# Kernel tuning notes

Measured on AMD Instinct MI355X. Metric: run time of the kernel, lower is better.

## Reference

```python
import jax, jax.numpy as jnp
import numpy as np

E = 32        # num_local_experts
TOP_K = 4     # num_experts_per_tok
H = 1024      # hidden_size
I = 1024      # intermediate_size (expert_dim)
ALPHA = 1.702
LIMIT = 7.0
B, S = 2, 1024


def setup_inputs() -> dict:
    key = jax.random.key(0)
    ks = jax.random.split(key, 8)
    scale = 0.02
    return {
        "hidden_states": jax.random.normal(ks[0], (B, S, H), dtype=jnp.float32),
        "gate_up_proj": jax.random.normal(ks[1], (E, H, 2 * I), dtype=jnp.float32) * scale,
        "gate_up_proj_bias": jax.random.normal(ks[2], (E, 2 * I), dtype=jnp.float32) * scale,
        "down_proj": jax.random.normal(ks[3], (E, I, H), dtype=jnp.float32) * scale,
        "down_proj_bias": jax.random.normal(ks[4], (E, H), dtype=jnp.float32) * scale,
        "router_weight": jax.random.normal(ks[5], (E, H), dtype=jnp.float32) * scale,
        "router_bias": jax.random.normal(ks[6], (E,), dtype=jnp.float32) * scale,
    }


def reference(hidden_states, gate_up_proj, gate_up_proj_bias, down_proj,
              down_proj_bias, router_weight, router_bias):
    b, s, h = hidden_states.shape
    x = hidden_states.reshape(-1, h)                       # [T, H], T = B*S
    t = x.shape[0]

    # ---- router: linear -> topk -> softmax over topk -> scatter to dense scores
    router_logits = x @ router_weight.T + router_bias      # [T, E]
    top_vals, top_idx = jax.lax.top_k(router_logits, TOP_K)
    top_w = jax.nn.softmax(top_vals, axis=-1)
    router_scores = jnp.zeros_like(router_logits).at[
        jnp.arange(t)[:, None], top_idx].set(top_w)        # [T, E]

    # ---- experts (dense all-expert path, interleaved gate/up columns)
    gate_w = gate_up_proj[..., 0::2]                       # [E, H, I]
    up_w = gate_up_proj[..., 1::2]                         # [E, H, I]
    gate_b = gate_up_proj_bias[..., 0::2]                  # [E, I]
    up_b = gate_up_proj_bias[..., 1::2]                    # [E, I]

    gate = jnp.einsum('th,ehi->eti', x, gate_w) + gate_b[:, None, :]
    up = jnp.einsum('th,ehi->eti', x, up_w) + up_b[:, None, :]
    gate = jnp.minimum(gate, LIMIT)
    up = jnp.clip(up, -LIMIT, LIMIT)
    glu = gate * jax.nn.sigmoid(gate * ALPHA)
    next_states = jnp.einsum('eti,eih->eth', (up + 1.0) * glu, down_proj)
    next_states = next_states + down_proj_bias[:, None, :]  # [E, T, H]

    # ---- combine: weight each expert output by its routing score and sum
    routed = jnp.einsum('eth,te->th', next_states, router_scores)
    return routed.reshape(b, s, h), router_scores
```

## Files before the change

kernel.cpp:

```cpp
#include <hip/hip_runtime.h>
#include <cstdint>
#include <cstddef>

#define E_ 32
#define TOPK_ 4
#define H_ 1024
#define I_ 1024
#define T_ 2048
#define ALPHA_ 1.702f
#define LIMIT_ 7.0f
#define TP_ 66
#define NCH_ 32

typedef __attribute__((ext_vector_type(8))) short s8;
typedef __attribute__((ext_vector_type(4))) float f4;

__device__ __forceinline__ unsigned short f2bf(float f) {
  unsigned int u = __float_as_uint(f);
  return (unsigned short)((u + 0x7fffu + ((u >> 16) & 1u)) >> 16);
}

__device__ __forceinline__ void gload_lds16(const unsigned short* g,
                                            unsigned short* l) {
  __builtin_amdgcn_global_load_lds(
      (const __attribute__((address_space(1))) void*)g,
      (__attribute__((address_space(3))) void*)l, 16, 0, 0);
}

__global__ __launch_bounds__(256)
void cast_x_kernel(const float* __restrict__ x, unsigned short* __restrict__ xb) {
  size_t i = (size_t)(blockIdx.x * 256 + threadIdx.x) * 8;
  float4 a = *(const float4*)(x + i);
  float4 b = *(const float4*)(x + i + 4);
  s8 v;
  v[0] = (short)f2bf(a.x); v[1] = (short)f2bf(a.y);
  v[2] = (short)f2bf(a.z); v[3] = (short)f2bf(a.w);
  v[4] = (short)f2bf(b.x); v[5] = (short)f2bf(b.y);
  v[6] = (short)f2bf(b.z); v[7] = (short)f2bf(b.w);
  *(s8*)(xb + i) = v;
}

__global__ __launch_bounds__(256)
void transpose_cast(const float* __restrict__ src, unsigned short* __restrict__ dst,
                    int src_rows, int src_cols, int deint) {
  int e = blockIdx.z;
  int c0 = blockIdx.x * 64;
  int r0 = blockIdx.y * 64;
  int tid = threadIdx.x;
  __shared__ unsigned short ldsT[64][TP_];

  const float* sp = src + (size_t)e * src_rows * src_cols
                        + (size_t)r0 * src_cols + c0;
  int r = tid >> 2, cq = tid & 3;
  const float* rowp = sp + (size_t)r * src_cols + cq * 4;
  #pragma unroll
  for (int j = 0; j < 4; ++j) {
    float4 v = *(const float4*)(rowp + j * 16);
    int c = cq * 4 + j * 16;
    ldsT[c + 0][r] = f2bf(v.x);
    ldsT[c + 1][r] = f2bf(v.y);
    ldsT[c + 2][r] = f2bf(v.z);
    ldsT[c + 3][r] = f2bf(v.w);
  }
  __syncthreads();

  int co = tid >> 2, hq = tid & 3;
  s8 v0 = *(s8*)&ldsT[co][hq * 16];
  s8 v1 = *(s8*)&ldsT[co][hq * 16 + 8];
  int C = c0 + co;
  size_t out_off;
  if (deint) {
    out_off = (size_t)e * src_cols * src_rows
            + (size_t)(C & 1) * (src_cols >> 1) * src_rows
            + (size_t)(C >> 1) * src_rows + r0 + hq * 16;
  } else {
    out_off = (size_t)e * src_cols * src_rows
            + (size_t)C * src_rows + r0 + hq * 16;
  }
  *(s8*)(dst + out_off) = v0;
  *(s8*)(dst + out_off + 8) = v1;
}

__global__ __launch_bounds__(128)
void router_kernel(const float* __restrict__ x,
                   const float* __restrict__ rw,
                   const float* __restrict__ rb,
                   float* __restrict__ scores,
                   int* __restrict__ counts,
                   int* __restrict__ tok_list,
                   float* __restrict__ w_list) {
  int t = blockIdx.x;
  int tid = threadIdx.x;
  __shared__ float partial[128];
  __shared__ float logits[E_];
  int e = tid & 31, q = tid >> 5;
  const float4* xp = (const float4*)(x + (size_t)t * H_ + q * 256);
  const float4* wp = (const float4*)(rw + (size_t)e * H_ + q * 256);
  float s = 0.f;
  #pragma unroll 8
  for (int h = 0; h < 64; ++h) {
    float4 a = xp[h], b = wp[h];
    s += a.x * b.x + a.y * b.y + a.z * b.z + a.w * b.w;
  }
  partial[tid] = s;
  __syncthreads();
  if (tid < 32)
    logits[tid] = partial[tid] + partial[tid + 32] + partial[tid + 64] +
                  partial[tid + 96] + rb[tid];
  __syncthreads();
  if (tid == 0) {
    float l[E_];
    #pragma unroll
    for (int i = 0; i < E_; ++i) l[i] = logits[i];
    int idx[TOPK_]; float v[TOPK_];
    for (int k = 0; k < TOPK_; ++k) {
      int bi = 0; float bv = -1e30f;
      for (int i = 0; i < E_; ++i)
        if (l[i] > bv) { bv = l[i]; bi = i; }
      idx[k] = bi; v[k] = bv; l[bi] = -1e30f;
    }
    float m = v[0], den = 0.f, w[TOPK_];
    for (int k = 0; k < TOPK_; ++k) { w[k] = expf(v[k] - m); den += w[k]; }
    float inv = 1.f / den;
    float* srow = scores + (size_t)t * E_;
    #pragma unroll
    for (int i = 0; i < E_; ++i) srow[i] = 0.f;
    for (int k = 0; k < TOPK_; ++k) {
      float wk = w[k] * inv;
      srow[idx[k]] = wk;
      int pos = atomicAdd(&counts[idx[k]], 1);
      tok_list[idx[k] * T_ + pos] = t * TOPK_ + k;
      w_list[idx[k] * T_ + pos] = wk;
    }
  }
}

__global__ __launch_bounds__(256)
void gateup_mfma(const unsigned short* __restrict__ xb,
                 const unsigned short* __restrict__ wgu,
                 const float* __restrict__ gb,
                 const int* __restrict__ counts,
                 const int* __restrict__ tok_list,
                 unsigned short* __restrict__ act) {
  int lid = blockIdx.x;
  int xcd = lid & 7, s = lid >> 3;
  int e = (xcd << 2) + (s >> 7);
  int w = s & 127;
  int tblk = w & 7;
  int itile = w >> 3;

  int cnt = counts[e];
  int t0 = tblk * 64;
  if (t0 >= cnt) return;
  int tid = threadIdx.x;
  int lane = tid & 63;
  int wave = tid >> 6;
  int wm = wave >> 1, wn = wave & 1;

  __shared__ __align__(16) unsigned short Xs[2][64][32];
  __shared__ __align__(16) unsigned short Wg[2][128][32];
  __shared__ int toks[64];

  if (tid < 64) {
    int slot = t0 + tid;
    toks[tid] = (slot < cnt) ? tok_list[e * T_ + slot] : -1;
  }
  __syncthreads();

  int fm = lane & 15, ko = (lane >> 4) * 8;
  f4 accg[2][2] = {};
  f4 accu[2][2] = {};

  int arow = (wave << 4) + (lane >> 2);
  int aenc_l = toks[arow];
  const unsigned short* srcA =
      xb + (size_t)((aenc_l < 0) ? 0 : (aenc_l >> 2)) * H_ + ((lane & 3) << 3);
  int br0 = (wave << 5) + (lane >> 2);
  int br1 = br0 + 16;
  size_t R0 = (br0 < 64) ? (size_t)(itile * 64 + br0)
                         : (size_t)(I_ + itile * 64 + (br0 - 64));
  size_t R1 = (br1 < 64) ? (size_t)(itile * 64 + br1)
                         : (size_t)(I_ + itile * 64 + (br1 - 64));
  const unsigned short* wbase = wgu + (size_t)e * 2 * I_ * H_ + ((lane & 3) << 3);
  const unsigned short* srcB0 = wbase + R0 * H_;
  const unsigned short* srcB1 = wbase + R1 * H_;

#define GU_ISSUE(CC, P)                                                      \
  {                                                                          \
    gload_lds16(srcA + (size_t)(CC) * 32, &Xs[P][wave << 4][0]);             \
    gload_lds16(srcB0 + (size_t)(CC) * 32, &Wg[P][wave << 5][0]);            \
    gload_lds16(srcB1 + (size_t)(CC) * 32, &Wg[P][(wave << 5) + 16][0]);     \
  }

  GU_ISSUE(0, 0)
  GU_ISSUE(1, 1)
  asm volatile("s_waitcnt vmcnt(3)" ::: "memory");
  __builtin_amdgcn_s_barrier();
  asm volatile("" ::: "memory");

  for (int c = 0; c < NCH_; ++c) {
    int P = c & 1;
    {
      s8 a0 = *(const s8*)&Xs[P][wm * 32 + fm][ko];
      s8 a1 = *(const s8*)&Xs[P][wm * 32 + 16 + fm][ko];
      #pragma unroll
      for (int g = 0; g < 2; ++g) {
        s8 bg = *(const s8*)&Wg[P][wn * 32 + g * 16 + fm][ko];
        s8 bu = *(const s8*)&Wg[P][64 + wn * 32 + g * 16 + fm][ko];
        accg[0][g] = __builtin_amdgcn_mfma_f32_16x16x32_bf16(a0, bg, accg[0][g], 0, 0, 0);
        accg[1][g] = __builtin_amdgcn_mfma_f32_16x16x32_bf16(a1, bg, accg[1][g], 0, 0, 0);
        accu[0][g] = __builtin_amdgcn_mfma_f32_16x16x32_bf16(a0, bu, accu[0][g], 0, 0, 0);
        accu[1][g] = __builtin_amdgcn_mfma_f32_16x16x32_bf16(a1, bu, accu[1][g], 0, 0, 0);
      }
    }
    __builtin_amdgcn_s_barrier();
    asm volatile("" ::: "memory");
    if (c < NCH_ - 2) {
      GU_ISSUE(c + 2, P)
      asm volatile("s_waitcnt vmcnt(3)" ::: "memory");
    } else if (c == NCH_ - 2) {
      asm volatile("s_waitcnt vmcnt(0)" ::: "memory");
    }
    __builtin_amdgcn_s_barrier();
    asm volatile("" ::: "memory");
  }
#undef GU_ISSUE

  int rq = lane >> 4;
  #pragma unroll
  for (int g = 0; g < 2; ++g) {
    int i = itile * 64 + wn * 32 + g * 16 + fm;
    float bg_ = gb[e * 2 * I_ + 2 * i];
    float bu_ = gb[e * 2 * I_ + 2 * i + 1];
    #pragma unroll
    for (int f = 0; f < 2; ++f) {
      #pragma unroll
      for (int r = 0; r < 4; ++r) {
        int m = wm * 32 + f * 16 + rq * 4 + r;
        int enc = toks[m];
        if (enc < 0) continue;
        float gv = accg[f][g][r] + bg_;
        float uv = accu[f][g][r] + bu_;
        gv = fminf(gv, LIMIT_);
        uv = fminf(fmaxf(uv, -LIMIT_), LIMIT_);
        float glu = gv / (1.f + __expf(-ALPHA_ * gv));
        act[(size_t)enc * I_ + i] = f2bf((uv + 1.f) * glu);
      }
    }
  }
}

__global__ __launch_bounds__(256)
void down_mfma(const unsigned short* __restrict__ act,
               const unsigned short* __restrict__ wdt,
               const float* __restrict__ db,
               const int* __restrict__ counts,
               const int* __restrict__ tok_list,
               const float* __restrict__ w_list,
               float* __restrict__ dsout) {
  int lid = blockIdx.x;
  int xcd = lid & 7, s = lid >> 3;
  int e = (xcd << 2) + (s >> 6);
  int w = s & 63;
  int tblk = w & 7;
  int htile = w >> 3;

  int cnt = counts[e];
  int t0 = tblk * 64;
  if (t0 >= cnt) return;
  int tid = threadIdx.x;
  int lane = tid & 63;
  int wave = tid >> 6;
  int wm = wave >> 1, wn = wave & 1;

  __shared__ __align__(16) unsigned short Xs[2][64][32];
  __shared__ __align__(16) unsigned short Wd[2][128][32];
  __shared__ int toks[64];
  __shared__ float tws[64];

  if (tid < 64) {
    int slot = t0 + tid;
    bool ok = slot < cnt;
    toks[tid] = ok ? tok_list[e * T_ + slot] : -1;
    tws[tid]  = ok ? w_list[e * T_ + slot] : 0.f;
  }
  __syncthreads();

  int fm = lane & 15, ko = (lane >> 4) * 8;
  f4 acc[2][4] = {};

  int arow = (wave << 4) + (lane >> 2);
  int aenc_l = toks[arow];
  const unsigned short* srcA =
      act + (size_t)((aenc_l < 0) ? 0 : aenc_l) * I_ + ((lane & 3) << 3);
  int br0 = (wave << 5) + (lane >> 2);
  int br1 = br0 + 16;
  const unsigned short* wbase = wdt + (size_t)e * H_ * I_ + ((lane & 3) << 3);
  const unsigned short* srcB0 = wbase + (size_t)(htile * 128 + br0) * I_;
  const unsigned short* srcB1 = wbase + (size_t)(htile * 128 + br1) * I_;

#define DN_ISSUE(CC, P)                                                      \
  {                                                                          \
    gload_lds16(srcA + (size_t)(CC) * 32, &Xs[P][wave << 4][0]);             \
    gload_lds16(srcB0 + (size_t)(CC) * 32, &Wd[P][wave << 5][0]);            \
    gload_lds16(srcB1 + (size_t)(CC) * 32, &Wd[P][(wave << 5) + 16][0]);     \
  }

  DN_ISSUE(0, 0)
  DN_ISSUE(1, 1)
  asm volatile("s_waitcnt vmcnt(3)" ::: "memory");
  __builtin_amdgcn_s_barrier();
  asm volatile("" ::: "memory");

  for (int c = 0; c < NCH_; ++c) {
    int P = c & 1;
    {
      s8 a0 = *(const s8*)&Xs[P][wm * 32 + fm][ko];
      s8 a1 = *(const s8*)&Xs[P][wm * 32 + 16 + fm][ko];
      #pragma unroll
      for (int g = 0; g < 4; ++g) {
        s8 b = *(const s8*)&Wd[P][wn * 64 + g * 16 + fm][ko];
        acc[0][g] = __builtin_amdgcn_mfma_f32_16x16x32_bf16(a0, b, acc[0][g], 0, 0, 0);
        acc[1][g] = __builtin_amdgcn_mfma_f32_16x16x32_bf16(a1, b, acc[1][g], 0, 0, 0);
      }
    }
    __builtin_amdgcn_s_barrier();
    asm volatile("" ::: "memory");
    if (c < NCH_ - 2) {
      DN_ISSUE(c + 2, P)
      asm volatile("s_waitcnt vmcnt(3)" ::: "memory");
    } else if (c == NCH_ - 2) {
      asm volatile("s_waitcnt vmcnt(0)" ::: "memory");
    }
    __builtin_amdgcn_s_barrier();
    asm volatile("" ::: "memory");
  }
#undef DN_ISSUE

  int rq = lane >> 4;
  #pragma unroll
  for (int g = 0; g < 4; ++g) {
    int h = htile * 128 + wn * 64 + g * 16 + fm;
    float bias = db[e * H_ + h];
    #pragma unroll
    for (int f = 0; f < 2; ++f) {
      #pragma unroll
      for (int r = 0; r < 4; ++r) {
        int m = wm * 32 + f * 16 + rq * 4 + r;
        int enc = toks[m];
        if (enc < 0) continue;
        dsout[(size_t)enc * H_ + h] = (acc[f][g][r] + bias) * tws[m];
      }
    }
  }
}

__global__ __launch_bounds__(256)
void combine_kernel(const float* __restrict__ dsout,
                    float* __restrict__ routed) {
  int idx = blockIdx.x * 256 + threadIdx.x;
  int t = idx >> 8;
  int h = (idx & 255) * 4;
  const float* base = dsout + (size_t)t * 4 * H_ + h;
  float4 a = *(const float4*)(base);
  float4 b = *(const float4*)(base + H_);
  float4 c = *(const float4*)(base + 2 * H_);
  float4 d = *(const float4*)(base + 3 * H_);
  float4 o;
  o.x = a.x + b.x + c.x + d.x;
  o.y = a.y + b.y + c.y + d.y;
  o.z = a.z + b.z + c.z + d.z;
  o.w = a.w + b.w + c.w + d.w;
  *(float4*)(routed + (size_t)t * H_ + h) = o;
}

extern "C" void kernel_launch(void* const* d_in, const int* in_sizes, int n_in,
                              void* d_out, int out_size, void* d_ws, size_t ws_size,
                              hipStream_t stream) {
  (void)in_sizes; (void)n_in; (void)out_size; (void)ws_size;
  const float* x    = (const float*)d_in[0];
  const float* gup  = (const float*)d_in[1];
  const float* gupb = (const float*)d_in[2];
  const float* dwn  = (const float*)d_in[3];
  const float* dwnb = (const float*)d_in[4];
  const float* rw   = (const float*)d_in[5];
  const float* rb   = (const float*)d_in[6];

  float* routed = (float*)d_out;
  float* scores = (float*)d_out + (size_t)T_ * H_;

  char* ws = (char*)d_ws;
  int*   counts   = (int*)ws;
  int*   tok_list = (int*)(ws + ((size_t)1 << 20));
  float* w_list   = (float*)(ws + ((size_t)1 << 20) + (size_t)E_ * T_ * 4);
  unsigned short* xbf = (unsigned short*)(ws + ((size_t)2 << 20));
  unsigned short* act = (unsigned short*)(ws + ((size_t)8 << 20));
  unsigned short* wgu_b = (unsigned short*)(ws + ((size_t)24 << 20));
  float*          dsout = (float*)(ws + ((size_t)24 << 20));
  unsigned short* wdt_b = (unsigned short*)(ws + ((size_t)24 << 20)
                                            + (size_t)E_ * 2 * I_ * H_ * 2);

  hipMemsetAsync(counts, 0, E_ * sizeof(int), stream);

  cast_x_kernel<<<(T_ * H_ / 8) / 256, 256, 0, stream>>>(x, xbf);
  transpose_cast<<<dim3(2 * I_ / 64, H_ / 64, E_), 256, 0, stream>>>(
      gup, wgu_b, H_, 2 * I_, 1);
  transpose_cast<<<dim3(H_ / 64, I_ / 64, E_), 256, 0, stream>>>(
      dwn, wdt_b, I_, H_, 0);
  router_kernel<<<T_, 128, 0, stream>>>(x, rw, rb, scores, counts, tok_list, w_list);
  gateup_mfma<<<4096, 256, 0, stream>>>(xbf, wgu_b, gupb, counts, tok_list, act);
  down_mfma<<<2048, 256, 0, stream>>>(act, wdt_b, dwnb, counts, tok_list,
                                      w_list, dsout);
  combine_kernel<<<(T_ * H_ / 4) / 256, 256, 0, stream>>>(dsout, routed);
}
```

Baseline: 738.0 us.

## Merge prep kernels, enlarge token tiles, swizzle LDS, atomically combine expert outputs

Router, x cast and both weight transposes now run as branches of a single prep kernel launch. The gate-up and down GEMMs use 128-token tiles instead of 64, with an XOR swizzle on LDS columns to reduce bank conflicts, and issue fewer blocks. The separate combine kernel is removed: the down kernel atomically adds weighted outputs into a zeroed output buffer. This cuts launch overhead and weight reloads, but adds atomic contention and makes the summation order nondeterministic. Also, with a max of 512 tokens per expert, any expert routed more than 512 tokens would be dropped.

```diff
diff --git a/kernel.cpp b/kernel.cpp
--- a/kernel.cpp
+++ b/kernel.cpp
@@ -12,6 +12,11 @@
 #define TP_ 66
 #define NCH_ 32
 
+#define NB_RTR_  2048
+#define NB_CAST_ 1024
+#define NB_TGUP_ 16384
+#define NB_TDWN_ 8192
+
 typedef __attribute__((ext_vector_type(8))) short s8;
 typedef __attribute__((ext_vector_type(4))) float f4;
 
@@ -27,28 +32,10 @@
       (__attribute__((address_space(3))) void*)l, 16, 0, 0);
 }
 
-__global__ __launch_bounds__(256)
-void cast_x_kernel(const float* __restrict__ x, unsigned short* __restrict__ xb) {
-  size_t i = (size_t)(blockIdx.x * 256 + threadIdx.x) * 8;
-  float4 a = *(const float4*)(x + i);
-  float4 b = *(const float4*)(x + i + 4);
-  s8 v;
-  v[0] = (short)f2bf(a.x); v[1] = (short)f2bf(a.y);
-  v[2] = (short)f2bf(a.z); v[3] = (short)f2bf(a.w);
-  v[4] = (short)f2bf(b.x); v[5] = (short)f2bf(b.y);
-  v[6] = (short)f2bf(b.z); v[7] = (short)f2bf(b.w);
-  *(s8*)(xb + i) = v;
-}
-
-__global__ __launch_bounds__(256)
-void transpose_cast(const float* __restrict__ src, unsigned short* __restrict__ dst,
-                    int src_rows, int src_cols, int deint) {
-  int e = blockIdx.z;
-  int c0 = blockIdx.x * 64;
-  int r0 = blockIdx.y * 64;
-  int tid = threadIdx.x;
-  __shared__ unsigned short ldsT[64][TP_];
-
+__device__ __forceinline__ void transpose_body(
+    const float* __restrict__ src, unsigned short* __restrict__ dst,
+    int src_rows, int src_cols, int deint, int e, int c0, int r0, int tid,
+    unsigned short (*ldsT)[TP_]) {
   const float* sp = src + (size_t)e * src_rows * src_cols
                         + (size_t)r0 * src_cols + c0;
   int r = tid >> 2, cq = tid & 3;
@@ -63,7 +50,6 @@
     ldsT[c + 3][r] = f2bf(v.w);
   }
   __syncthreads();
-
   int co = tid >> 2, hq = tid & 3;
   s8 v0 = *(s8*)&ldsT[co][hq * 16];
   s8 v1 = *(s8*)&ldsT[co][hq * 16 + 8];
@@ -81,57 +67,99 @@
   *(s8*)(dst + out_off + 8) = v1;
 }
 
-__global__ __launch_bounds__(128)
-void router_kernel(const float* __restrict__ x,
-                   const float* __restrict__ rw,
-                   const float* __restrict__ rb,
-                   float* __restrict__ scores,
-                   int* __restrict__ counts,
-                   int* __restrict__ tok_list,
-                   float* __restrict__ w_list) {
-  int t = blockIdx.x;
+__global__ __launch_bounds__(256)
+void prep_kernel(const float* __restrict__ x,
+                 const float* __restrict__ rw,
+                 const float* __restrict__ rb,
+                 const float* __restrict__ gup,
+                 const float* __restrict__ dwn,
+                 float* __restrict__ scores,
+                 int* __restrict__ counts,
+                 int* __restrict__ tok_list,
+                 float* __restrict__ w_list,
+                 unsigned short* __restrict__ xbf,
+                 unsigned short* __restrict__ wgu_b,
+                 unsigned short* __restrict__ wdt_b) {
+  __shared__ __align__(16) char smem[64 * TP_ * 2];
+  int bid = blockIdx.x;
   int tid = threadIdx.x;
-  __shared__ float partial[128];
-  __shared__ float logits[E_];
-  int e = tid & 31, q = tid >> 5;
-  const float4* xp = (const float4*)(x + (size_t)t * H_ + q * 256);
-  const float4* wp = (const float4*)(rw + (size_t)e * H_ + q * 256);
-  float s = 0.f;
-  #pragma unroll 8
-  for (int h = 0; h < 64; ++h) {
-    float4 a = xp[h], b = wp[h];
-    s += a.x * b.x + a.y * b.y + a.z * b.z + a.w * b.w;
-  }
-  partial[tid] = s;
-  __syncthreads();
-  if (tid < 32)
-    logits[tid] = partial[tid] + partial[tid + 32] + partial[tid + 64] +
-                  partial[tid + 96] + rb[tid];
-  __syncthreads();
-  if (tid == 0) {
-    float l[E_];
-    #pragma unroll
-    for (int i = 0; i < E_; ++i) l[i] = logits[i];
-    int idx[TOPK_]; float v[TOPK_];
-    for (int k = 0; k < TOPK_; ++k) {
-      int bi = 0; float bv = -1e30f;
-      for (int i = 0; i < E_; ++i)
-        if (l[i] > bv) { bv = l[i]; bi = i; }
-      idx[k] = bi; v[k] = bv; l[bi] = -1e30f;
-    }
-    float m = v[0], den = 0.f, w[TOPK_];
-    for (int k = 0; k < TOPK_; ++k) { w[k] = expf(v[k] - m); den += w[k]; }
-    float inv = 1.f / den;
-    float* srow = scores + (size_t)t * E_;
-    #pragma unroll
-    for (int i = 0; i < E_; ++i) srow[i] = 0.f;
-    for (int k = 0; k < TOPK_; ++k) {
-      float wk = w[k] * inv;
-      srow[idx[k]] = wk;
-      int pos = atomicAdd(&counts[idx[k]], 1);
-      tok_list[idx[k] * T_ + pos] = t * TOPK_ + k;
-      w_list[idx[k] * T_ + pos] = wk;
-    }
+
+  if (bid < NB_RTR_) {
+    float* partial = (float*)smem;
+    float* logits  = partial + 256;
+    int t = bid;
+    int e = tid & 31, q = tid >> 5;
+    const float4* xp = (const float4*)(x + (size_t)t * H_ + q * 128);
+    const float4* wp = (const float4*)(rw + (size_t)e * H_ + q * 128);
+    float s = 0.f;
+    #pragma unroll 8
+    for (int h = 0; h < 32; ++h) {
+      float4 a = xp[h], b = wp[h];
+      s += a.x * b.x + a.y * b.y + a.z * b.z + a.w * b.w;
+    }
+    partial[tid] = s;
+    __syncthreads();
+    if (tid < 32) {
+      float acc = 0.f;
+      #pragma unroll
+      for (int j = 0; j < 8; ++j) acc += partial[j * 32 + tid];
+      logits[tid] = acc + rb[tid];
+    }
+    __syncthreads();
+    if (tid == 0) {
+      float l[E_];
+      #pragma unroll
+      for (int i = 0; i < E_; ++i) l[i] = logits[i];
+      int idx[TOPK_]; float v[TOPK_];
+      for (int k = 0; k < TOPK_; ++k) {
+        int bi = 0; float bv = -1e30f;
+        #pragma unroll
+        for (int i = 0; i < E_; ++i)
+          if (l[i] > bv) { bv = l[i]; bi = i; }
+        idx[k] = bi; v[k] = bv; l[bi] = -1e30f;
+      }
+      float m = v[0], den = 0.f, w[TOPK_];
+      #pragma unroll
+      for (int k = 0; k < TOPK_; ++k) { w[k] = expf(v[k] - m); den += w[k]; }
+      float inv = 1.f / den;
+      float* srow = scores + (size_t)t * E_;
+      #pragma unroll
+      for (int i = 0; i < E_; ++i) srow[i] = 0.f;
+      for (int k = 0; k < TOPK_; ++k) {
+        float wk = w[k] * inv;
+        srow[idx[k]] = wk;
+        int pos = atomicAdd(&counts[idx[k]], 1);
+        tok_list[idx[k] * T_ + pos] = t * TOPK_ + k;
+        w_list[idx[k] * T_ + pos] = wk;
+      }
+    }
+  } else if (bid < NB_RTR_ + NB_CAST_) {
+    int b2 = bid - NB_RTR_;
+    size_t i = (size_t)(b2 * 256 + tid) * 8;
+    float4 a = *(const float4*)(x + i);
+    float4 b = *(const float4*)(x + i + 4);
+    s8 v;
+    v[0] = (short)f2bf(a.x); v[1] = (short)f2bf(a.y);
+    v[2] = (short)f2bf(a.z); v[3] = (short)f2bf(a.w);
+    v[4] = (short)f2bf(b.x); v[5] = (short)f2bf(b.y);
+    v[6] = (short)f2bf(b.z); v[7] = (short)f2bf(b.w);
+    *(s8*)(xbf + i) = v;
+  } else if (bid < NB_RTR_ + NB_CAST_ + NB_TGUP_) {
+    int b3 = bid - (NB_RTR_ + NB_CAST_);
+    int e = b3 >> 9;
+    int rem = b3 & 511;
+    int c0 = (rem & 31) * 64;
+    int r0 = (rem >> 5) * 64;
+    transpose_body(gup, wgu_b, H_, 2 * I_, 1, e, c0, r0, tid,
+                   (unsigned short (*)[TP_])smem);
+  } else {
+    int b4 = bid - (NB_RTR_ + NB_CAST_ + NB_TGUP_);
+    int e = b4 >> 8;
+    int rem = b4 & 255;
+    int c0 = (rem & 15) * 64;
+    int r0 = (rem >> 4) * 64;
+    transpose_body(dwn, wdt_b, I_, H_, 0, e, c0, r0, tid,
+                   (unsigned short (*)[TP_])smem);
   }
 }
 
@@ -144,80 +172,102 @@
                  unsigned short* __restrict__ act) {
   int lid = blockIdx.x;
   int xcd = lid & 7, s = lid >> 3;
-  int e = (xcd << 2) + (s >> 7);
-  int w = s & 127;
-  int tblk = w & 7;
-  int itile = w >> 3;
+  int e = (xcd << 2) + (s >> 6);
+  int rem = s & 63;
+  int itile = rem >> 2;
+  int tb = rem & 3;
 
   int cnt = counts[e];
-  int t0 = tblk * 64;
+  int t0 = tb * 128;
   if (t0 >= cnt) return;
   int tid = threadIdx.x;
   int lane = tid & 63;
   int wave = tid >> 6;
   int wm = wave >> 1, wn = wave & 1;
 
-  __shared__ __align__(16) unsigned short Xs[2][64][32];
+  __shared__ __align__(16) unsigned short Xs[2][128][32];
   __shared__ __align__(16) unsigned short Wg[2][128][32];
-  __shared__ int toks[64];
-
-  if (tid < 64) {
+  __shared__ int toks[128];
+
+  if (tid < 128) {
     int slot = t0 + tid;
     toks[tid] = (slot < cnt) ? tok_list[e * T_ + slot] : -1;
   }
   __syncthreads();
 
-  int fm = lane & 15, ko = (lane >> 4) * 8;
-  f4 accg[2][2] = {};
-  f4 accu[2][2] = {};
-
-  int arow = (wave << 4) + (lane >> 2);
-  int aenc_l = toks[arow];
-  const unsigned short* srcA =
-      xb + (size_t)((aenc_l < 0) ? 0 : (aenc_l >> 2)) * H_ + ((lane & 3) << 3);
-  int br0 = (wave << 5) + (lane >> 2);
-  int br1 = br0 + 16;
-  size_t R0 = (br0 < 64) ? (size_t)(itile * 64 + br0)
-                         : (size_t)(I_ + itile * 64 + (br0 - 64));
-  size_t R1 = (br1 < 64) ? (size_t)(itile * 64 + br1)
-                         : (size_t)(I_ + itile * 64 + (br1 - 64));
-  const unsigned short* wbase = wgu + (size_t)e * 2 * I_ * H_ + ((lane & 3) << 3);
-  const unsigned short* srcB0 = wbase + R0 * H_;
-  const unsigned short* srcB1 = wbase + R1 * H_;
+  int fm = lane & 15;
+  int kc = lane >> 4;
+  f4 accg[4][2] = {};
+  f4 accu[4][2] = {};
+
+  int srow0 = (wave << 5) + (lane >> 2);
+  int srow1 = srow0 + 16;
+  int sc0 = ((lane & 3) ^ ((srow0 >> 1) & 3)) << 3;
+  int sc1 = ((lane & 3) ^ ((srow1 >> 1) & 3)) << 3;
+  int enc0 = toks[srow0], enc1 = toks[srow1];
+  const unsigned short* srcA0 =
+      xb + (size_t)((enc0 < 0) ? 0 : (enc0 >> 2)) * H_ + sc0;
+  const unsigned short* srcA1 =
+      xb + (size_t)((enc1 < 0) ? 0 : (enc1 >> 2)) * H_ + sc1;
+  size_t R0 = (srow0 < 64) ? (size_t)(itile * 64 + srow0)
+                           : (size_t)(I_ + itile * 64 + (srow0 - 64));
+  size_t R1 = (srow1 < 64) ? (size_t)(itile * 64 + srow1)
+                           : (size_t)(I_ + itile * 64 + (srow1 - 64));
+  const unsigned short* wbase = wgu + (size_t)e * 2 * I_ * H_;
+  const unsigned short* srcB0 = wbase + R0 * H_ + sc0;
+  const unsigned short* srcB1 = wbase + R1 * H_ + sc1;
+
+  int ar[4], ac[4];
+  #pragma unroll
+  for (int f = 0; f < 4; ++f) {
+    int r = wm * 64 + f * 16 + fm;
+    ar[f] = r;
+    ac[f] = (kc ^ ((r >> 1) & 3)) << 3;
+  }
+  int brg[2], bcg[2];
+  #pragma unroll
+  for (int g = 0; g < 2; ++g) {
+    int r = wn * 32 + g * 16 + fm;
+    brg[g] = r;
+    bcg[g] = (kc ^ ((r >> 1) & 3)) << 3;
+  }
 
 #define GU_ISSUE(CC, P)                                                      \
   {                                                                          \
-    gload_lds16(srcA + (size_t)(CC) * 32, &Xs[P][wave << 4][0]);             \
-    gload_lds16(srcB0 + (size_t)(CC) * 32, &Wg[P][wave << 5][0]);            \
+    gload_lds16(srcA0 + (size_t)(CC) * 32, &Xs[P][(wave << 5)][0]);          \
+    gload_lds16(srcA1 + (size_t)(CC) * 32, &Xs[P][(wave << 5) + 16][0]);     \
+    gload_lds16(srcB0 + (size_t)(CC) * 32, &Wg[P][(wave << 5)][0]);          \
     gload_lds16(srcB1 + (size_t)(CC) * 32, &Wg[P][(wave << 5) + 16][0]);     \
   }
 
   GU_ISSUE(0, 0)
   GU_ISSUE(1, 1)
-  asm volatile("s_waitcnt vmcnt(3)" ::: "memory");
+  asm volatile("s_waitcnt vmcnt(4)" ::: "memory");
   __builtin_amdgcn_s_barrier();
   asm volatile("" ::: "memory");
 
   for (int c = 0; c < NCH_; ++c) {
     int P = c & 1;
     {
-      s8 a0 = *(const s8*)&Xs[P][wm * 32 + fm][ko];
-      s8 a1 = *(const s8*)&Xs[P][wm * 32 + 16 + fm][ko];
+      s8 a[4];
+      #pragma unroll
+      for (int f = 0; f < 4; ++f) a[f] = *(const s8*)&Xs[P][ar[f]][ac[f]];
       #pragma unroll
       for (int g = 0; g < 2; ++g) {
-        s8 bg = *(const s8*)&Wg[P][wn * 32 + g * 16 + fm][ko];
-        s8 bu = *(const s8*)&Wg[P][64 + wn * 32 + g * 16 + fm][ko];
-        accg[0][g] = __builtin_amdgcn_mfma_f32_16x16x32_bf16(a0, bg, accg[0][g], 0, 0, 0);
-        accg[1][g] = __builtin_amdgcn_mfma_f32_16x16x32_bf16(a1, bg, accg[1][g], 0, 0, 0);
-        accu[0][g] = __builtin_amdgcn_mfma_f32_16x16x32_bf16(a0, bu, accu[0][g], 0, 0, 0);
-        accu[1][g] = __builtin_amdgcn_mfma_f32_16x16x32_bf16(a1, bu, accu[1][g], 0, 0, 0);
+        s8 bg = *(const s8*)&Wg[P][brg[g]][bcg[g]];
+        s8 bu = *(const s8*)&Wg[P][64 + brg[g]][bcg[g]];
+        #pragma unroll
+        for (int f = 0; f < 4; ++f) {
+          accg[f][g] = __builtin_amdgcn_mfma_f32_16x16x32_bf16(a[f], bg, accg[f][g], 0, 0, 0);
+          accu[f][g] = __builtin_amdgcn_mfma_f32_16x16x32_bf16(a[f], bu, accu[f][g], 0, 0, 0);
+        }
       }
     }
     __builtin_amdgcn_s_barrier();
     asm volatile("" ::: "memory");
     if (c < NCH_ - 2) {
       GU_ISSUE(c + 2, P)
-      asm volatile("s_waitcnt vmcnt(3)" ::: "memory");
+      asm volatile("s_waitcnt vmcnt(4)" ::: "memory");
     } else if (c == NCH_ - 2) {
       asm volatile("s_waitcnt vmcnt(0)" ::: "memory");
     }
@@ -233,10 +283,10 @@
     float bg_ = gb[e * 2 * I_ + 2 * i];
     float bu_ = gb[e * 2 * I_ + 2 * i + 1];
     #pragma unroll
-    for (int f = 0; f < 2; ++f) {
+    for (int f = 0; f < 4; ++f) {
       #pragma unroll
       for (int r = 0; r < 4; ++r) {
-        int m = wm * 32 + f * 16 + rq * 4 + r;
+        int m = wm * 64 + f * 16 + rq * 4 + r;
         int enc = toks[m];
         if (enc < 0) continue;
         float gv = accg[f][g][r] + bg_;
@@ -257,28 +307,28 @@
                const int* __restrict__ counts,
                const int* __restrict__ tok_list,
                const float* __restrict__ w_list,
-               float* __restrict__ dsout) {
+               float* __restrict__ routed) {
   int lid = blockIdx.x;
   int xcd = lid & 7, s = lid >> 3;
-  int e = (xcd << 2) + (s >> 6);
-  int w = s & 63;
-  int tblk = w & 7;
-  int htile = w >> 3;
+  int e = (xcd << 2) + (s >> 5);
+  int rem = s & 31;
+  int htile = rem >> 2;
+  int tb = rem & 3;
 
   int cnt = counts[e];
-  int t0 = tblk * 64;
+  int t0 = tb * 128;
   if (t0 >= cnt) return;
   int tid = threadIdx.x;
   int lane = tid & 63;
   int wave = tid >> 6;
   int wm = wave >> 1, wn = wave & 1;
 
-  __shared__ __align__(16) unsigned short Xs[2][64][32];
+  __shared__ __align__(16) unsigned short Xs[2][128][32];
   __shared__ __align__(16) unsigned short Wd[2][128][32];
-  __shared__ int toks[64];
-  __shared__ float tws[64];
-
-  if (tid < 64) {
+  __shared__ int toks[128];
+  __shared__ float tws[128];
+
+  if (tid < 128) {
     int slot = t0 + tid;
     bool ok = slot < cnt;
     toks[tid] = ok ? tok_list[e * T_ + slot] : -1;
@@ -286,49 +336,71 @@
   }
   __syncthreads();
 
-  int fm = lane & 15, ko = (lane >> 4) * 8;
-  f4 acc[2][4] = {};
-
-  int arow = (wave << 4) + (lane >> 2);
-  int aenc_l = toks[arow];
-  const unsigned short* srcA =
-      act + (size_t)((aenc_l < 0) ? 0 : aenc_l) * I_ + ((lane & 3) << 3);
-  int br0 = (wave << 5) + (lane >> 2);
-  int br1 = br0 + 16;
-  const unsigned short* wbase = wdt + (size_t)e * H_ * I_ + ((lane & 3) << 3);
-  const unsigned short* srcB0 = wbase + (size_t)(htile * 128 + br0) * I_;
-  const unsigned short* srcB1 = wbase + (size_t)(htile * 128 + br1) * I_;
+  int fm = lane & 15;
+  int kc = lane >> 4;
+  f4 acc[4][4] = {};
+
+  int srow0 = (wave << 5) + (lane >> 2);
+  int srow1 = srow0 + 16;
+  int sc0 = ((lane & 3) ^ ((srow0 >> 1) & 3)) << 3;
+  int sc1 = ((lane & 3) ^ ((srow1 >> 1) & 3)) << 3;
+  int enc0 = toks[srow0], enc1 = toks[srow1];
+  const unsigned short* srcA0 =
+      act + (size_t)((enc0 < 0) ? 0 : enc0) * I_ + sc0;
+  const unsigned short* srcA1 =
+      act + (size_t)((enc1 < 0) ? 0 : enc1) * I_ + sc1;
+  const unsigned short* wbase = wdt + (size_t)e * H_ * I_;
+  const unsigned short* srcB0 = wbase + (size_t)(htile * 128 + srow0) * I_ + sc0;
+  const unsigned short* srcB1 = wbase + (size_t)(htile * 128 + srow1) * I_ + sc1;
+
+  int ar[4], ac_[4];
+  #pragma unroll
+  for (int f = 0; f < 4; ++f) {
+    int r = wm * 64 + f * 16 + fm;
+    ar[f] = r;
+    ac_[f] = (kc ^ ((r >> 1) & 3)) << 3;
+  }
+  int brg[4], bcg[4];
+  #pragma unroll
+  for (int g = 0; g < 4; ++g) {
+    int r = wn * 64 + g * 16 + fm;
+    brg[g] = r;
+    bcg[g] = (kc ^ ((r >> 1) & 3)) << 3;
+  }
 
 #define DN_ISSUE(CC, P)                                                      \
   {                                                                          \
-    gload_lds16(srcA + (size_t)(CC) * 32, &Xs[P][wave << 4][0]);             \
-    gload_lds16(srcB0 + (size_t)(CC) * 32, &Wd[P][wave << 5][0]);            \
+    gload_lds16(srcA0 + (size_t)(CC) * 32, &Xs[P][(wave << 5)][0]);          \
+    gload_lds16(srcA1 + (size_t)(CC) * 32, &Xs[P][(wave << 5) + 16][0]);     \
+    gload_lds16(srcB0 + (size_t)(CC) * 32, &Wd[P][(wave << 5)][0]);          \
     gload_lds16(srcB1 + (size_t)(CC) * 32, &Wd[P][(wave << 5) + 16][0]);     \
   }
 
   DN_ISSUE(0, 0)
   DN_ISSUE(1, 1)
-  asm volatile("s_waitcnt vmcnt(3)" ::: "memory");
+  asm volatile("s_waitcnt vmcnt(4)" ::: "memory");
   __builtin_amdgcn_s_barrier();
   asm volatile("" ::: "memory");
 
   for (int c = 0; c < NCH_; ++c) {
     int P = c & 1;
     {
-      s8 a0 = *(const s8*)&Xs[P][wm * 32 + fm][ko];
-      s8 a1 = *(const s8*)&Xs[P][wm * 32 + 16 + fm][ko];
+      s8 a[4];
+      #pragma unroll
+      for (int f = 0; f < 4; ++f) a[f] = *(const s8*)&Xs[P][ar[f]][ac_[f]];
       #pragma unroll
       for (int g = 0; g < 4; ++g) {
-        s8 b = *(const s8*)&Wd[P][wn * 64 + g * 16 + fm][ko];
-        acc[0][g] = __builtin_amdgcn_mfma_f32_16x16x32_bf16(a0, b, acc[0][g], 0, 0, 0);
-        acc[1][g] = __builtin_amdgcn_mfma_f32_16x16x32_bf16(a1, b, acc[1][g], 0, 0, 0);
+        s8 b = *(const s8*)&Wd[P][brg[g]][bcg[g]];
+        #pragma unroll
+        for (int f = 0; f < 4; ++f)
+          acc[f][g] = __builtin_amdgcn_mfma_f32_16x16x32_bf16(a[f], b, acc[f][g], 0, 0, 0);
       }
     }
     __builtin_amdgcn_s_barrier();
     asm volatile("" ::: "memory");
     if (c < NCH_ - 2) {
       DN_ISSUE(c + 2, P)
-      asm volatile("s_waitcnt vmcnt(3)" ::: "memory");
+      asm volatile("s_waitcnt vmcnt(4)" ::: "memory");
     } else if (c == NCH_ - 2) {
       asm volatile("s_waitcnt vmcnt(0)" ::: "memory");
     }
@@ -343,35 +415,17 @@
     int h = htile * 128 + wn * 64 + g * 16 + fm;
     float bias = db[e * H_ + h];
     #pragma unroll
-    for (int f = 0; f < 2; ++f) {
+    for (int f = 0; f < 4; ++f) {
       #pragma unroll
       for (int r = 0; r < 4; ++r) {
-        int m = wm * 32 + f * 16 + rq * 4 + r;
+        int m = wm * 64 + f * 16 + rq * 4 + r;
         int enc = toks[m];
         if (enc < 0) continue;
-        dsout[(size_t)enc * H_ + h] = (acc[f][g][r] + bias) * tws[m];
-      }
-    }
-  }
-}
-
-__global__ __launch_bounds__(256)
-void combine_kernel(const float* __restrict__ dsout,
-                    float* __restrict__ routed) {
-  int idx = blockIdx.x * 256 + threadIdx.x;
-  int t = idx >> 8;
-  int h = (idx & 255) * 4;
-  const float* base = dsout + (size_t)t * 4 * H_ + h;
-  float4 a = *(const float4*)(base);
-  float4 b = *(const float4*)(base + H_);
-  float4 c = *(const float4*)(base + 2 * H_);
-  float4 d = *(const float4*)(base + 3 * H_);
-  float4 o;
-  o.x = a.x + b.x + c.x + d.x;
-  o.y = a.y + b.y + c.y + d.y;
-  o.z = a.z + b.z + c.z + d.z;
-  o.w = a.w + b.w + c.w + d.w;
-  *(float4*)(routed + (size_t)t * H_ + h) = o;
+        atomicAdd(&routed[(size_t)(enc >> 2) * H_ + h],
+                  (acc[f][g][r] + bias) * tws[m]);
+      }
+    }
+  }
 }
 
 extern "C" void kernel_launch(void* const* d_in, const int* in_sizes, int n_in,
@@ -396,20 +450,15 @@
   unsigned short* xbf = (unsigned short*)(ws + ((size_t)2 << 20));
   unsigned short* act = (unsigned short*)(ws + ((size_t)8 << 20));
   unsigned short* wgu_b = (unsigned short*)(ws + ((size_t)24 << 20));
-  float*          dsout = (float*)(ws + ((size_t)24 << 20));
   unsigned short* wdt_b = (unsigned short*)(ws + ((size_t)24 << 20)
                                             + (size_t)E_ * 2 * I_ * H_ * 2);
 
   hipMemsetAsync(counts, 0, E_ * sizeof(int), stream);
-
-  cast_x_kernel<<<(T_ * H_ / 8) / 256, 256, 0, stream>>>(x, xbf);
-  transpose_cast<<<dim3(2 * I_ / 64, H_ / 64, E_), 256, 0, stream>>>(
-      gup, wgu_b, H_, 2 * I_, 1);
-  transpose_cast<<<dim3(H_ / 64, I_ / 64, E_), 256, 0, stream>>>(
-      dwn, wdt_b, I_, H_, 0);
-  router_kernel<<<T_, 128, 0, stream>>>(x, rw, rb, scores, counts, tok_list, w_list);
-  gateup_mfma<<<4096, 256, 0, stream>>>(xbf, wgu_b, gupb, counts, tok_list, act);
-  down_mfma<<<2048, 256, 0, stream>>>(act, wdt_b, dwnb, counts, tok_list,
-                                      w_list, dsout);
-  combine_kernel<<<(T_ * H_ / 4) / 256, 256, 0, stream>>>(dsout, routed);
-}
+  hipMemsetAsync(routed, 0, (size_t)T_ * H_ * sizeof(float), stream);
+
+  prep_kernel<<<NB_RTR_ + NB_CAST_ + NB_TGUP_ + NB_TDWN_, 256, 0, stream>>>(
+      x, rw, rb, gup, dwn, scores, counts, tok_list, w_list, xbf, wgu_b, wdt_b);
+  gateup_mfma<<<2048, 256, 0, stream>>>(xbf, wgu_b, gupb, counts, tok_list, act);
+  down_mfma<<<1024, 256, 0, stream>>>(act, wdt_b, dwnb, counts, tok_list,
+                                      w_list, routed);
+}
```

After: 751.5 us. No clear change (+1.8%).
